# Kernel tuning notes

Hardware: AMD Instinct MI355X
Metric: run time of the kernel (lower is better)

## Reference

```python
import jax, jax.numpy as jnp
import numpy as np

LEAKY_SLOPE = 0.01  # torch nn.LeakyReLU default

def leaky_relu(x):
    return jnp.where(x >= 0, x, LEAKY_SLOPE * x)

def setup_inputs() -> dict:
    key = jax.random.key(0)
    ks = jax.random.split(key, 11)
    B, F, C_IN, H, K, D = 2048, 512, 3, 64, 8, 128  # batch, features, expand, layer_conf[0], bucket_num, bucket_dim
    ASR, MM, OUT = 128, 768, 256
    proj_in = ASR + MM + F * D
    inp = {
        "stat_features": jax.random.uniform(ks[0], (B, F), dtype=jnp.float32),
        "asr_embeddings": jax.random.normal(ks[1], (B, ASR), dtype=jnp.float32),
        "mm_embeddings": jax.random.normal(ks[2], (B, MM), dtype=jnp.float32),
        "linear1_w": jax.random.normal(ks[3], (F, C_IN, H), dtype=jnp.float32) * (1.0 / np.sqrt(C_IN)),
        "linear1_b": jax.random.normal(ks[4], (F, 1, H), dtype=jnp.float32),
        "linear2_w": jax.random.normal(ks[5], (F, H, K), dtype=jnp.float32) * (1.0 / np.sqrt(H)),
        "linear2_b": jax.random.normal(ks[6], (F, 1, K), dtype=jnp.float32),
        "tau": jnp.ones((F, 1, K), dtype=jnp.float32),
        "emb": jax.random.normal(ks[7], (F, K, D), dtype=jnp.float32),
        "proj_w": jax.random.normal(ks[8], (OUT, proj_in), dtype=jnp.float32) * (1.0 / np.sqrt(proj_in)),
        "proj_b": jax.random.normal(ks[9], (OUT,), dtype=jnp.float32) * 0.01,
    }
    return inp

def reference(stat_features, asr_embeddings, mm_embeddings,
              linear1_w, linear1_b, linear2_w, linear2_b, tau, emb,
              proj_w, proj_b):
    # sanitize: NaN -> 0, negatives -> 0
    x = stat_features
    x = jnp.where(jnp.isnan(x) | (x < 0.0), 0.0, x)  # [B, F]

    # auto_dis: per-feature tiny MLP. x is expanded to 3 identical copies -> [B,F,1,3]
    # matmul with [F,3,H] == einsum over the 3 copies.
    B, F = x.shape
    x3 = jnp.broadcast_to(x[:, :, None], (B, F, 3))           # [B,F,3]
    h = jnp.einsum('bfc,fch->bfh', x3, linear1_w) + linear1_b[:, 0, :]  # [B,F,H]
    h = jnp.where(h >= 0, h, LEAKY_SLOPE * h)
    s = jnp.einsum('bfh,fhk->bfk', h, linear2_w) + linear2_b[:, 0, :]   # [B,F,K]
    s = jnp.where(s >= 0, s, LEAKY_SLOPE * s)
    s = s * tau[:, 0, :]
    p = jax.nn.softmax(s, axis=-1)                            # [B,F,K]
    y = jnp.einsum('bfk,fkd->bfd', p, emb)                    # [B,F,D]
    y = y.reshape(B, -1)                                      # [B, F*D] (fc = Identity)

    z = jnp.concatenate([asr_embeddings, mm_embeddings, y], axis=1)
    out = jax.nn.relu(z @ proj_w.T + proj_b)                  # [B, 256]
    return out
```

## Files before the change

kernel.cpp:

```cpp
#include <hip/hip_runtime.h>
#include <hip/hip_bf16.h>
#include <math.h>

#define LEAKY 0.01f
#define B_    2048
#define F_    512
#define H_    64
#define K_    8
#define D_    128
#define ASR_  128
#define MM_   768
#define OUT_  256
#define PROJ_IN 66432
#define ZK    4992
#define PK    4096


typedef unsigned short u16;
typedef u16   u16x4 __attribute__((ext_vector_type(4)));
typedef u16   u16x8 __attribute__((ext_vector_type(8)));
typedef short s16x8 __attribute__((ext_vector_type(8)));
typedef float f32x4 __attribute__((ext_vector_type(4)));

__device__ __forceinline__ u16 f2bf(float x) {
  unsigned int u = __float_as_uint(x);
  u += 0x7fffu + ((u >> 16) & 1u);
  return (u16)(u >> 16);
}

#define W1S 65
#define W2S 516
__global__ __launch_bounds__(256) void probs_kernel(
    const float* __restrict__ stat, const float* __restrict__ w1,
    const float* __restrict__ b1v, const float* __restrict__ w2,
    const float* __restrict__ b2v, const float* __restrict__ tauv,
    u16* __restrict__ P) {
  const int f0 = blockIdx.x * 8;
  const int b0 = blockIdx.y * 256;
  __shared__ float s_w1s[8 * W1S], s_b1[8 * W1S];
  __shared__ float s_w2[8 * W2S];
  __shared__ float s_b2[64], s_tau[64];
  __shared__ float s_x[256 * 8];
  const int t = threadIdx.x;
  for (int i = t; i < 8 * 64; i += 256) {
    int fl = i >> 6, h = i & 63;
    const float* wf = w1 + (size_t)(f0 + fl) * 192;
    s_w1s[fl * W1S + h] = wf[h] + wf[64 + h] + wf[128 + h];
    s_b1[fl * W1S + h] = b1v[(size_t)(f0 + fl) * 64 + h];
  }
  for (int i = t; i < 8 * 512; i += 256) {
    int fl = i >> 9, idx = i & 511;
    s_w2[fl * W2S + idx] = w2[(size_t)(f0 + fl) * 512 + idx];
  }
  if (t < 64) {
    int fl = t >> 3, k = t & 7;
    s_b2[t]  = b2v[(f0 + fl) * 8 + k];
    s_tau[t] = tauv[(f0 + fl) * 8 + k];
  }
  for (int i = t; i < 2048; i += 256) {
    int r = i >> 3, j = i & 7;
    float v = stat[(size_t)(b0 + r) * F_ + f0 + j];
    s_x[i] = (v >= 0.f) ? v : 0.f;
  }
  __syncthreads();

  const int fl = t & 7, rb = t >> 3;
  float x[8];
  #pragma unroll
  for (int p = 0; p < 8; ++p) x[p] = s_x[(rb + 32 * p) * 8 + fl];
  float acc[8][8] = {{0.f}};
  const float* w1p = s_w1s + fl * W1S;
  const float* b1p = s_b1 + fl * W1S;
  const float* w2p = s_w2 + fl * W2S;
  #pragma unroll 8
  for (int i = 0; i < 64; ++i) {
    float wv = w1p[i], bv = b1p[i];
    float4 wa = *(const float4*)(w2p + i * 8);
    float4 wb = *(const float4*)(w2p + i * 8 + 4);
    #pragma unroll
    for (int p = 0; p < 8; ++p) {
      float h = fmaf(x[p], wv, bv);
      h = (h >= 0.f) ? h : LEAKY * h;
      acc[p][0] = fmaf(h, wa.x, acc[p][0]);
      acc[p][1] = fmaf(h, wa.y, acc[p][1]);
      acc[p][2] = fmaf(h, wa.z, acc[p][2]);
      acc[p][3] = fmaf(h, wa.w, acc[p][3]);
      acc[p][4] = fmaf(h, wb.x, acc[p][4]);
      acc[p][5] = fmaf(h, wb.y, acc[p][5]);
      acc[p][6] = fmaf(h, wb.z, acc[p][6]);
      acc[p][7] = fmaf(h, wb.w, acc[p][7]);
    }
  }
  #pragma unroll
  for (int p = 0; p < 8; ++p) {
    float s[K_];
    float m = -1e30f;
    #pragma unroll
    for (int k = 0; k < K_; ++k) {
      float v = acc[p][k] + s_b2[fl * 8 + k];
      v = (v >= 0.f) ? v : LEAKY * v;
      v *= s_tau[fl * 8 + k];
      s[k] = v;
      m = fmaxf(m, v);
    }
    float sum = 0.f;
    #pragma unroll
    for (int k = 0; k < K_; ++k) { s[k] = __expf(s[k] - m); sum += s[k]; }
    float inv = 1.f / sum;
    u16x8 hv;
    #pragma unroll
    for (int k = 0; k < K_; ++k) hv[k] = f2bf(s[k] * inv);
    *(u16x8*)(P + (size_t)(b0 + rb + 32 * p) * PK + (f0 + fl) * 8) = hv;
  }
}

__global__ __launch_bounds__(256) void wn_top_kernel(
    const float* __restrict__ pw, u16* __restrict__ Wn) {
  int idx = blockIdx.x * 256 + threadIdx.x;
  if (idx >= OUT_ * 896) return;
  int o = idx / 896, j = idx % 896;
  Wn[(size_t)o * ZK + j] = f2bf(pw[(size_t)o * PROJ_IN + j]);
}

__global__ __launch_bounds__(256) void wn_g_kernel(
    const float* __restrict__ pw, const float* __restrict__ emb,
    u16* __restrict__ Wn) {
  const int f = blockIdx.x;
  const int o0 = blockIdx.y * 64;
  __shared__ float s_emb[K_ * D_];
  const int t = threadIdx.x;
  for (int i = t; i < K_ * D_; i += 256) s_emb[i] = emb[(size_t)f * K_ * D_ + i];
  __syncthreads();
  const int orow = t >> 2, dc = t & 3;
  const float* src = pw + (size_t)(o0 + orow) * PROJ_IN + 896 + f * D_;
  float g[K_] = {0.f, 0.f, 0.f, 0.f, 0.f, 0.f, 0.f, 0.f};
  #pragma unroll
  for (int j = 0; j < 8; ++j) {
    const int d = dc * 4 + j * 16;
    float4 w = *(const float4*)(src + d);
    #pragma unroll
    for (int k = 0; k < K_; ++k) {
      float4 e = *(const float4*)(s_emb + k * D_ + d);
      g[k] = fmaf(w.x, e.x, g[k]);
      g[k] = fmaf(w.y, e.y, g[k]);
      g[k] = fmaf(w.z, e.z, g[k]);
      g[k] = fmaf(w.w, e.w, g[k]);
    }
  }
  #pragma unroll
  for (int k = 0; k < K_; ++k) {
    g[k] += __shfl_xor(g[k], 1);
    g[k] += __shfl_xor(g[k], 2);
  }
  if (dc == 0) {
    u16x8 hv;
    #pragma unroll
    for (int k = 0; k < K_; ++k) hv[k] = f2bf(g[k]);
    *(u16x8*)(Wn + (size_t)(o0 + orow) * ZK + 896 + f * K_) = hv;
  }
}

#define SAS 136
__global__ __launch_bounds__(256) void gemm_kernel(
    const float* __restrict__ asr, const float* __restrict__ mm,
    const u16* __restrict__ P, const u16* __restrict__ Wn,
    const float* __restrict__ bias, float* __restrict__ out) {
  const int bm0 = blockIdx.x * 32;
  const int bn0 = blockIdx.y * 32;
  __shared__ u16 sA[32 * SAS];
  __shared__ u16 sB[32 * SAS];
  const int t = threadIdx.x;
  const int w = t >> 6, L = t & 63;
  const int l16 = L & 15, q8 = (L >> 4) * 8;
  const int mrow = (w >> 1) * 16, ncol = (w & 1) * 16;
  const int row = t >> 3, lk = t & 7;
  f32x4 acc = {0.f, 0.f, 0.f, 0.f};

  float4 fa[4];
  u16x8 pa[2];
  u16x8 wb[2];

#define LOAD_TILES(IT)                                                        \
  {                                                                           \
    const int k0_ = (IT) * 128;                                               \
    if ((IT) == 0) {                                                          \
      const float* s_ = asr + (size_t)(bm0 + row) * ASR_ + lk * 4;            \
      fa[0] = *(const float4*)(s_);                                           \
      fa[1] = *(const float4*)(s_ + 32);                                      \
      fa[2] = *(const float4*)(s_ + 64);                                      \
      fa[3] = *(const float4*)(s_ + 96);                                      \
    } else if ((IT) < 7) {                                                    \
      const float* s_ = mm + (size_t)(bm0 + row) * MM_ + (k0_ - 128) + lk * 4;\
      fa[0] = *(const float4*)(s_);                                           \
      fa[1] = *(const float4*)(s_ + 32);                                      \
      fa[2] = *(const float4*)(s_ + 64);                                      \
      fa[3] = *(const float4*)(s_ + 96);                                      \
    } else {                                                                  \
      const u16* s_ = P + (size_t)(bm0 + row) * PK + (k0_ - 896) + lk * 8;    \
      pa[0] = *(const u16x8*)(s_);                                            \
      pa[1] = *(const u16x8*)(s_ + 64);                                       \
    }                                                                         \
    const u16* sb_ = Wn + (size_t)(bn0 + row) * ZK + k0_ + lk * 8;            \
    wb[0] = *(const u16x8*)(sb_);                                             \
    wb[1] = *(const u16x8*)(sb_ + 64);                                        \
  }

#define STORE_TILES(IT)                                                       \
  {                                                                           \
    if ((IT) < 7) {                                                           \
      _Pragma("unroll")                                                       \
      for (int j_ = 0; j_ < 4; ++j_) {                                        \
        u16x4 h_ = {f2bf(fa[j_].x), f2bf(fa[j_].y), f2bf(fa[j_].z),           \
                    f2bf(fa[j_].w)};                                          \
        *(u16x4*)&sA[row * SAS + lk * 4 + j_ * 32] = h_;                      \
      }                                                                       \
    } else {                                                                  \
      *(u16x8*)&sA[row * SAS + lk * 8] = pa[0];                               \
      *(u16x8*)&sA[row * SAS + lk * 8 + 64] = pa[1];                          \
    }                                                                         \
    *(u16x8*)&sB[row * SAS + lk * 8] = wb[0];                                 \
    *(u16x8*)&sB[row * SAS + lk * 8 + 64] = wb[1];                            \
  }

  LOAD_TILES(0);
  for (int it = 0; it < 39; ++it) {
    __syncthreads();
    STORE_TILES(it);
    __syncthreads();
    if (it < 38) LOAD_TILES(it + 1);
    #pragma unroll
    for (int ks = 0; ks < 4; ++ks) {
      s16x8 a = *(const s16x8*)&sA[(mrow + l16) * SAS + ks * 32 + q8];
      s16x8 b = *(const s16x8*)&sB[(ncol + l16) * SAS + ks * 32 + q8];
      acc = __builtin_amdgcn_mfma_f32_16x16x32_bf16(a, b, acc, 0, 0, 0);
    }
  }
#undef LOAD_TILES
#undef STORE_TILES

  const int col = bn0 + ncol + l16;
  const float bv = bias[col];
  const int r0 = bm0 + mrow + (L >> 4) * 4;
  #pragma unroll
  for (int i = 0; i < 4; ++i) {
    float v = acc[i] + bv;
    out[(size_t)(r0 + i) * OUT_ + col] = v > 0.f ? v : 0.f;
  }
}

extern "C" void kernel_launch(void* const* d_in, const int* in_sizes, int n_in,
                              void* d_out, int out_size, void* d_ws, size_t ws_size,
                              hipStream_t stream) {
  (void)in_sizes; (void)n_in; (void)out_size; (void)ws_size;
  const float* stat = (const float*)d_in[0];
  const float* asr  = (const float*)d_in[1];
  const float* mm   = (const float*)d_in[2];
  const float* w1   = (const float*)d_in[3];
  const float* b1   = (const float*)d_in[4];
  const float* w2   = (const float*)d_in[5];
  const float* b2   = (const float*)d_in[6];
  const float* tau  = (const float*)d_in[7];
  const float* emb  = (const float*)d_in[8];
  const float* pw   = (const float*)d_in[9];
  const float* pb   = (const float*)d_in[10];
  float* out = (float*)d_out;
  char* ws = (char*)d_ws;
  u16* P  = (u16*)(ws);
  u16* Wn = (u16*)(ws + 16777216);

  probs_kernel<<<dim3(F_ / 8, B_ / 256), 256, 0, stream>>>(stat, w1, b1, w2, b2, tau, P);
  wn_top_kernel<<<(OUT_ * 896 + 255) / 256, 256, 0, stream>>>(pw, Wn);
  wn_g_kernel<<<dim3(F_, 4), 256, 0, stream>>>(pw, emb, Wn);
  gemm_kernel<<<dim3(B_ / 32, OUT_ / 32), 256, 0, stream>>>(asr, mm, P, Wn, pb, out);
}
```

Baseline: 180.3 us.

## Merge producer kernels into one launch and split GEMM K across four blocks

Combines the probability kernel and both weight-folding kernels into one producer launch that dispatches on block index, so there is one launch and the branches run concurrently. The GEMM is split along K into four slices writing fp32 partial sums to workspace, and a new combine kernel adds the slices, the bias and the ReLU. The intent is to raise GEMM occupancy beyond the 512-block grid and shorten each block's serial K loop. The cost is extra partial-sum traffic (four B×OUT fp32 buffers) and one extra launch.

```diff
diff --git a/kernel.cpp b/kernel.cpp
--- a/kernel.cpp
+++ b/kernel.cpp
@@ -14,6 +14,7 @@
 #define PROJ_IN 66432
 #define ZK    4992
 #define PK    4096
+#define NSPLIT 4
 
 
 typedef unsigned short u16;
@@ -30,133 +31,139 @@
 
 #define W1S 65
 #define W2S 516
-__global__ __launch_bounds__(256) void probs_kernel(
+#define PRODUCER_BLOCKS (512 + 2048 + 224)
+
+__global__ __launch_bounds__(256) void producer_kernel(
     const float* __restrict__ stat, const float* __restrict__ w1,
     const float* __restrict__ b1v, const float* __restrict__ w2,
     const float* __restrict__ b2v, const float* __restrict__ tauv,
-    u16* __restrict__ P) {
-  const int f0 = blockIdx.x * 8;
-  const int b0 = blockIdx.y * 256;
-  __shared__ float s_w1s[8 * W1S], s_b1[8 * W1S];
-  __shared__ float s_w2[8 * W2S];
-  __shared__ float s_b2[64], s_tau[64];
-  __shared__ float s_x[256 * 8];
+    const float* __restrict__ pw, const float* __restrict__ emb,
+    u16* __restrict__ P, u16* __restrict__ Wn) {
+  __shared__ __align__(16) char smem[29376];
+  const int bid = blockIdx.x;
   const int t = threadIdx.x;
-  for (int i = t; i < 8 * 64; i += 256) {
-    int fl = i >> 6, h = i & 63;
-    const float* wf = w1 + (size_t)(f0 + fl) * 192;
-    s_w1s[fl * W1S + h] = wf[h] + wf[64 + h] + wf[128 + h];
-    s_b1[fl * W1S + h] = b1v[(size_t)(f0 + fl) * 64 + h];
-  }
-  for (int i = t; i < 8 * 512; i += 256) {
-    int fl = i >> 9, idx = i & 511;
-    s_w2[fl * W2S + idx] = w2[(size_t)(f0 + fl) * 512 + idx];
-  }
-  if (t < 64) {
-    int fl = t >> 3, k = t & 7;
-    s_b2[t]  = b2v[(f0 + fl) * 8 + k];
-    s_tau[t] = tauv[(f0 + fl) * 8 + k];
-  }
-  for (int i = t; i < 2048; i += 256) {
-    int r = i >> 3, j = i & 7;
-    float v = stat[(size_t)(b0 + r) * F_ + f0 + j];
-    s_x[i] = (v >= 0.f) ? v : 0.f;
-  }
-  __syncthreads();
-
-  const int fl = t & 7, rb = t >> 3;
-  float x[8];
-  #pragma unroll
-  for (int p = 0; p < 8; ++p) x[p] = s_x[(rb + 32 * p) * 8 + fl];
-  float acc[8][8] = {{0.f}};
-  const float* w1p = s_w1s + fl * W1S;
-  const float* b1p = s_b1 + fl * W1S;
-  const float* w2p = s_w2 + fl * W2S;
-  #pragma unroll 8
-  for (int i = 0; i < 64; ++i) {
-    float wv = w1p[i], bv = b1p[i];
-    float4 wa = *(const float4*)(w2p + i * 8);
-    float4 wb = *(const float4*)(w2p + i * 8 + 4);
+
+  if (bid < 512) {
+    const int f0 = (bid & 63) * 8;
+    const int b0 = (bid >> 6) * 256;
+    float* s_w1s = (float*)(smem);
+    float* s_b1  = (float*)(smem + 2080);
+    float* s_w2  = (float*)(smem + 4160);
+    float* s_b2  = (float*)(smem + 20672);
+    float* s_tau = (float*)(smem + 20928);
+    float* s_x   = (float*)(smem + 21184);
+    for (int i = t; i < 8 * 64; i += 256) {
+      int fl = i >> 6, h = i & 63;
+      const float* wf = w1 + (size_t)(f0 + fl) * 192;
+      s_w1s[fl * W1S + h] = wf[h] + wf[64 + h] + wf[128 + h];
+      s_b1[fl * W1S + h] = b1v[(size_t)(f0 + fl) * 64 + h];
+    }
+    for (int i = t; i < 8 * 512; i += 256) {
+      int fl = i >> 9, idx = i & 511;
+      s_w2[fl * W2S + idx] = w2[(size_t)(f0 + fl) * 512 + idx];
+    }
+    if (t < 64) {
+      int fl = t >> 3, k = t & 7;
+      s_b2[t]  = b2v[(f0 + fl) * 8 + k];
+      s_tau[t] = tauv[(f0 + fl) * 8 + k];
+    }
+    for (int i = t; i < 2048; i += 256) {
+      int r = i >> 3, j = i & 7;
+      float v = stat[(size_t)(b0 + r) * F_ + f0 + j];
+      s_x[i] = (v >= 0.f) ? v : 0.f;
+    }
+    __syncthreads();
+
+    const int fl = t & 7, rb = t >> 3;
+    float x[8];
+    #pragma unroll
+    for (int p = 0; p < 8; ++p) x[p] = s_x[(rb + 32 * p) * 8 + fl];
+    float acc[8][8] = {{0.f}};
+    const float* w1p = s_w1s + fl * W1S;
+    const float* b1p = s_b1 + fl * W1S;
+    const float* w2p = s_w2 + fl * W2S;
+    #pragma unroll 8
+    for (int i = 0; i < 64; ++i) {
+      float wv = w1p[i], bv = b1p[i];
+      float4 wa = *(const float4*)(w2p + i * 8);
+      float4 wb = *(const float4*)(w2p + i * 8 + 4);
+      #pragma unroll
+      for (int p = 0; p < 8; ++p) {
+        float h = fmaf(x[p], wv, bv);
+        h = (h >= 0.f) ? h : LEAKY * h;
+        acc[p][0] = fmaf(h, wa.x, acc[p][0]);
+        acc[p][1] = fmaf(h, wa.y, acc[p][1]);
+        acc[p][2] = fmaf(h, wa.z, acc[p][2]);
+        acc[p][3] = fmaf(h, wa.w, acc[p][3]);
+        acc[p][4] = fmaf(h, wb.x, acc[p][4]);
+        acc[p][5] = fmaf(h, wb.y, acc[p][5]);
+        acc[p][6] = fmaf(h, wb.z, acc[p][6]);
+        acc[p][7] = fmaf(h, wb.w, acc[p][7]);
+      }
+    }
     #pragma unroll
     for (int p = 0; p < 8; ++p) {
-      float h = fmaf(x[p], wv, bv);
-      h = (h >= 0.f) ? h : LEAKY * h;
-      acc[p][0] = fmaf(h, wa.x, acc[p][0]);
-      acc[p][1] = fmaf(h, wa.y, acc[p][1]);
-      acc[p][2] = fmaf(h, wa.z, acc[p][2]);
-      acc[p][3] = fmaf(h, wa.w, acc[p][3]);
-      acc[p][4] = fmaf(h, wb.x, acc[p][4]);
-      acc[p][5] = fmaf(h, wb.y, acc[p][5]);
-      acc[p][6] = fmaf(h, wb.z, acc[p][6]);
-      acc[p][7] = fmaf(h, wb.w, acc[p][7]);
-    }
-  }
-  #pragma unroll
-  for (int p = 0; p < 8; ++p) {
-    float s[K_];
-    float m = -1e30f;
+      float s[K_];
+      float m = -1e30f;
+      #pragma unroll
+      for (int k = 0; k < K_; ++k) {
+        float v = acc[p][k] + s_b2[fl * 8 + k];
+        v = (v >= 0.f) ? v : LEAKY * v;
+        v *= s_tau[fl * 8 + k];
+        s[k] = v;
+        m = fmaxf(m, v);
+      }
+      float sum = 0.f;
+      #pragma unroll
+      for (int k = 0; k < K_; ++k) { s[k] = __expf(s[k] - m); sum += s[k]; }
+      float inv = 1.f / sum;
+      u16x8 hv;
+      #pragma unroll
+      for (int k = 0; k < K_; ++k) hv[k] = f2bf(s[k] * inv);
+      *(u16x8*)(P + (size_t)(b0 + rb + 32 * p) * PK + (f0 + fl) * 8) = hv;
+    }
+  } else if (bid < 2560) {
+    const int item = bid - 512;
+    const int f = item >> 2;
+    const int o0 = (item & 3) * 64;
+    float* s_emb = (float*)smem;
+    for (int i = t; i < K_ * D_; i += 256) s_emb[i] = emb[(size_t)f * K_ * D_ + i];
+    __syncthreads();
+    const int orow = t >> 2, dc = t & 3;
+    const float* src = pw + (size_t)(o0 + orow) * PROJ_IN + 896 + f * D_;
+    float g[K_] = {0.f, 0.f, 0.f, 0.f, 0.f, 0.f, 0.f, 0.f};
+    #pragma unroll
+    for (int j = 0; j < 8; ++j) {
+      const int d = dc * 4 + j * 16;
+      float4 w = *(const float4*)(src + d);
+      #pragma unroll
+      for (int k = 0; k < K_; ++k) {
+        float4 e = *(const float4*)(s_emb + k * D_ + d);
+        g[k] = fmaf(w.x, e.x, g[k]);
+        g[k] = fmaf(w.y, e.y, g[k]);
+        g[k] = fmaf(w.z, e.z, g[k]);
+        g[k] = fmaf(w.w, e.w, g[k]);
+      }
+    }
     #pragma unroll
     for (int k = 0; k < K_; ++k) {
-      float v = acc[p][k] + s_b2[fl * 8 + k];
-      v = (v >= 0.f) ? v : LEAKY * v;
-      v *= s_tau[fl * 8 + k];
-      s[k] = v;
-      m = fmaxf(m, v);
-    }
-    float sum = 0.f;
-    #pragma unroll
-    for (int k = 0; k < K_; ++k) { s[k] = __expf(s[k] - m); sum += s[k]; }
-    float inv = 1.f / sum;
-    u16x8 hv;
-    #pragma unroll
-    for (int k = 0; k < K_; ++k) hv[k] = f2bf(s[k] * inv);
-    *(u16x8*)(P + (size_t)(b0 + rb + 32 * p) * PK + (f0 + fl) * 8) = hv;
-  }
-}
-
-__global__ __launch_bounds__(256) void wn_top_kernel(
-    const float* __restrict__ pw, u16* __restrict__ Wn) {
-  int idx = blockIdx.x * 256 + threadIdx.x;
-  if (idx >= OUT_ * 896) return;
-  int o = idx / 896, j = idx % 896;
-  Wn[(size_t)o * ZK + j] = f2bf(pw[(size_t)o * PROJ_IN + j]);
-}
-
-__global__ __launch_bounds__(256) void wn_g_kernel(
-    const float* __restrict__ pw, const float* __restrict__ emb,
-    u16* __restrict__ Wn) {
-  const int f = blockIdx.x;
-  const int o0 = blockIdx.y * 64;
-  __shared__ float s_emb[K_ * D_];
-  const int t = threadIdx.x;
-  for (int i = t; i < K_ * D_; i += 256) s_emb[i] = emb[(size_t)f * K_ * D_ + i];
-  __syncthreads();
-  const int orow = t >> 2, dc = t & 3;
-  const float* src = pw + (size_t)(o0 + orow) * PROJ_IN + 896 + f * D_;
-  float g[K_] = {0.f, 0.f, 0.f, 0.f, 0.f, 0.f, 0.f, 0.f};
-  #pragma unroll
-  for (int j = 0; j < 8; ++j) {
-    const int d = dc * 4 + j * 16;
-    float4 w = *(const float4*)(src + d);
-    #pragma unroll
-    for (int k = 0; k < K_; ++k) {
-      float4 e = *(const float4*)(s_emb + k * D_ + d);
-      g[k] = fmaf(w.x, e.x, g[k]);
-      g[k] = fmaf(w.y, e.y, g[k]);
-      g[k] = fmaf(w.z, e.z, g[k]);
-      g[k] = fmaf(w.w, e.w, g[k]);
-    }
-  }
-  #pragma unroll
-  for (int k = 0; k < K_; ++k) {
-    g[k] += __shfl_xor(g[k], 1);
-    g[k] += __shfl_xor(g[k], 2);
-  }
-  if (dc == 0) {
-    u16x8 hv;
-    #pragma unroll
-    for (int k = 0; k < K_; ++k) hv[k] = f2bf(g[k]);
-    *(u16x8*)(Wn + (size_t)(o0 + orow) * ZK + 896 + f * K_) = hv;
+      g[k] += __shfl_xor(g[k], 1);
+      g[k] += __shfl_xor(g[k], 2);
+    }
+    if (dc == 0) {
+      u16x8 hv;
+      #pragma unroll
+      for (int k = 0; k < K_; ++k) hv[k] = f2bf(g[k]);
+      *(u16x8*)(Wn + (size_t)(o0 + orow) * ZK + 896 + f * K_) = hv;
+    }
+  } else {
+    const int item = bid - 2560;
+    #pragma unroll
+    for (int r = 0; r < 4; ++r) {
+      int idx = item * 1024 + r * 256 + t;
+      int o = idx / 896, j = idx % 896;
+      Wn[(size_t)o * ZK + j] = f2bf(pw[(size_t)o * PROJ_IN + j]);
+    }
   }
 }
 
@@ -164,9 +171,12 @@
 __global__ __launch_bounds__(256) void gemm_kernel(
     const float* __restrict__ asr, const float* __restrict__ mm,
     const u16* __restrict__ P, const u16* __restrict__ Wn,
-    const float* __restrict__ bias, float* __restrict__ out) {
+    float* __restrict__ part) {
   const int bm0 = blockIdx.x * 32;
   const int bn0 = blockIdx.y * 32;
+  const int kz  = blockIdx.z;
+  const int it0 = kz * 10;
+  const int itn = (kz == 3) ? 9 : 10;
   __shared__ u16 sA[32 * SAS];
   __shared__ u16 sB[32 * SAS];
   const int t = threadIdx.x;
@@ -183,13 +193,13 @@
 #define LOAD_TILES(IT)                                                        \
   {                                                                           \
     const int k0_ = (IT) * 128;                                               \
-    if ((IT) == 0) {                                                          \
+    if (k0_ == 0) {                                                           \
       const float* s_ = asr + (size_t)(bm0 + row) * ASR_ + lk * 4;            \
       fa[0] = *(const float4*)(s_);                                           \
       fa[1] = *(const float4*)(s_ + 32);                                      \
       fa[2] = *(const float4*)(s_ + 64);                                      \
       fa[3] = *(const float4*)(s_ + 96);                                      \
-    } else if ((IT) < 7) {                                                    \
+    } else if (k0_ < 896) {                                                   \
       const float* s_ = mm + (size_t)(bm0 + row) * MM_ + (k0_ - 128) + lk * 4;\
       fa[0] = *(const float4*)(s_);                                           \
       fa[1] = *(const float4*)(s_ + 32);                                      \
@@ -207,7 +217,7 @@
 
 #define STORE_TILES(IT)                                                       \
   {                                                                           \
-    if ((IT) < 7) {                                                           \
+    if ((IT) * 128 < 896) {                                                   \
       _Pragma("unroll")                                                       \
       for (int j_ = 0; j_ < 4; ++j_) {                                        \
         u16x4 h_ = {f2bf(fa[j_].x), f2bf(fa[j_].y), f2bf(fa[j_].z),           \
@@ -222,12 +232,12 @@
     *(u16x8*)&sB[row * SAS + lk * 8 + 64] = wb[1];                            \
   }
 
-  LOAD_TILES(0);
-  for (int it = 0; it < 39; ++it) {
+  LOAD_TILES(it0);
+  for (int it = it0; it < it0 + itn; ++it) {
     __syncthreads();
     STORE_TILES(it);
     __syncthreads();
-    if (it < 38) LOAD_TILES(it + 1);
+    if (it + 1 < it0 + itn) LOAD_TILES(it + 1);
     #pragma unroll
     for (int ks = 0; ks < 4; ++ks) {
       s16x8 a = *(const s16x8*)&sA[(mrow + l16) * SAS + ks * 32 + q8];
@@ -239,13 +249,33 @@
 #undef STORE_TILES
 
   const int col = bn0 + ncol + l16;
-  const float bv = bias[col];
   const int r0 = bm0 + mrow + (L >> 4) * 4;
+  float* dst = part + (size_t)kz * B_ * OUT_;
   #pragma unroll
-  for (int i = 0; i < 4; ++i) {
-    float v = acc[i] + bv;
-    out[(size_t)(r0 + i) * OUT_ + col] = v > 0.f ? v : 0.f;
-  }
+  for (int i = 0; i < 4; ++i)
+    dst[(size_t)(r0 + i) * OUT_ + col] = acc[i];
+}
+
+__global__ __launch_bounds__(256) void combine_kernel(
+    const float* __restrict__ part, const float* __restrict__ pb,
+    float* __restrict__ out) {
+  const int idx4 = (blockIdx.x * 256 + threadIdx.x) * 4;
+  const int o = idx4 & (OUT_ - 1);
+  float4 a0 = *(const float4*)(part + idx4);
+  float4 a1 = *(const float4*)(part + (size_t)B_ * OUT_ + idx4);
+  float4 a2 = *(const float4*)(part + (size_t)2 * B_ * OUT_ + idx4);
+  float4 a3 = *(const float4*)(part + (size_t)3 * B_ * OUT_ + idx4);
+  float4 bv = *(const float4*)(pb + o);
+  float4 r;
+  r.x = a0.x + a1.x + a2.x + a3.x + bv.x;
+  r.y = a0.y + a1.y + a2.y + a3.y + bv.y;
+  r.z = a0.z + a1.z + a2.z + a3.z + bv.z;
+  r.w = a0.w + a1.w + a2.w + a3.w + bv.w;
+  r.x = r.x > 0.f ? r.x : 0.f;
+  r.y = r.y > 0.f ? r.y : 0.f;
+  r.z = r.z > 0.f ? r.z : 0.f;
+  r.w = r.w > 0.f ? r.w : 0.f;
+  *(float4*)(out + idx4) = r;
 }
 
 extern "C" void kernel_launch(void* const* d_in, const int* in_sizes, int n_in,
@@ -265,11 +295,13 @@
   const float* pb   = (const float*)d_in[10];
   float* out = (float*)d_out;
   char* ws = (char*)d_ws;
-  u16* P  = (u16*)(ws);
-  u16* Wn = (u16*)(ws + 16777216);
-
-  probs_kernel<<<dim3(F_ / 8, B_ / 256), 256, 0, stream>>>(stat, w1, b1, w2, b2, tau, P);
-  wn_top_kernel<<<(OUT_ * 896 + 255) / 256, 256, 0, stream>>>(pw, Wn);
-  wn_g_kernel<<<dim3(F_, 4), 256, 0, stream>>>(pw, emb, Wn);
-  gemm_kernel<<<dim3(B_ / 32, OUT_ / 32), 256, 0, stream>>>(asr, mm, P, Wn, pb, out);
-}
+  u16*   P    = (u16*)(ws);
+  u16*   Wn   = (u16*)(ws + 16777216);
+  float* part = (float*)(ws + 19333120);
+
+  producer_kernel<<<PRODUCER_BLOCKS, 256, 0, stream>>>(
+      stat, w1, b1, w2, b2, tau, pw, emb, P, Wn);
+  gemm_kernel<<<dim3(B_ / 32, OUT_ / 32, NSPLIT), 256, 0, stream>>>(
+      asr, mm, P, Wn, part);
+  combine_kernel<<<B_ * OUT_ / 1024, 256, 0, stream>>>(part, pb, out);
+}
```

After: 167.1 us. -7.4%, faster.
